# Optimization experiments

Measured on AMD Instinct MI355X. Metric: run time of the kernel, lower is better.

Reference implementation:

```python
import jax, jax.numpy as jnp
import numpy as np

SET_NUM, SET_SIZE, C, H, F, L_LAYERS, N_BLOCKS = 2048, 36, 192, 8, 384, 8, 4
N = SET_NUM * SET_SIZE


def _ln(x, g, b, eps=1e-5):
    m = x.mean(-1, keepdims=True)
    v = ((x - m) ** 2).mean(-1, keepdims=True)
    return (x - m) * jax.lax.rsqrt(v + eps) * g + b


def setup_inputs() -> dict:
    key = jax.random.key(0)
    ks = jax.random.split(key, 32)
    src = jax.random.normal(ks[0], (N, C), dtype=jnp.float32)
    pos_embed = jax.random.normal(ks[1], (2, N, C), dtype=jnp.float32)
    # each (shift, set) index tensor is a permutation of arange(N) -> every voxel appears exactly once
    perms = [jax.random.permutation(ks[2 + j], N).reshape(SET_NUM, SET_SIZE) for j in range(4)]
    set_voxel_inds = jnp.stack([jnp.stack(perms[0:2]), jnp.stack(perms[2:4])]).astype(jnp.int32)
    set_voxel_masks = jnp.zeros((2, 2, SET_NUM, SET_SIZE), dtype=bool)

    def p(k, shape, std=0.02):
        return (jax.random.normal(k, shape) * std).astype(jnp.float32)

    inp = dict(src=src, pos_embed=pos_embed, set_voxel_inds=set_voxel_inds,
               set_voxel_masks=set_voxel_masks,
               in_proj_w=p(ks[6], (L_LAYERS, 3 * C, C)), in_proj_b=p(ks[7], (L_LAYERS, 3 * C)),
               out_w=p(ks[8], (L_LAYERS, C, C)), out_b=p(ks[9], (L_LAYERS, C)),
               lin1_w=p(ks[10], (L_LAYERS, F, C)), lin1_b=p(ks[11], (L_LAYERS, F)),
               lin2_w=p(ks[12], (L_LAYERS, C, F)), lin2_b=p(ks[13], (L_LAYERS, C)),
               ln1_g=jnp.ones((L_LAYERS, C)), ln1_b=jnp.zeros((L_LAYERS, C)),
               ln2_g=jnp.ones((L_LAYERS, C)), ln2_b=jnp.zeros((L_LAYERS, C)),
               enc_g=jnp.ones((L_LAYERS, C)), enc_b=jnp.zeros((L_LAYERS, C)),
               blk_g=jnp.ones((N_BLOCKS, C)), blk_b=jnp.zeros((N_BLOCKS, C)))
    return inp


def reference(src, pos_embed, set_voxel_inds, set_voxel_masks,
              in_proj_w, in_proj_b, out_w, out_b, lin1_w, lin1_b, lin2_w, lin2_b,
              ln1_g, ln1_b, ln2_g, ln2_b, enc_g, enc_b, blk_g, blk_b):
    n_vox = src.shape[0]
    Dh = C // H
    scale = 1.0 / np.sqrt(Dh)

    def set_attn(x, pos, inds, mask, li):
        g = x[inds]                      # (S,K,C) gather voxels into sets
        qk_in = g + pos[inds]
        Wq, Wk, Wv = jnp.split(in_proj_w[li], 3, axis=0)
        bq, bk, bv = jnp.split(in_proj_b[li], 3)
        S, K = inds.shape
        q = (qk_in @ Wq.T + bq).reshape(S, K, H, Dh)
        k = (qk_in @ Wk.T + bk).reshape(S, K, H, Dh)
        v = (g @ Wv.T + bv).reshape(S, K, H, Dh)
        scores = jnp.einsum('skhd,slhd->shkl', q, k) * scale
        scores = jnp.where(mask[:, None, None, :], -1e9, scores)
        attn = jax.nn.softmax(scores, axis=-1)
        o = jnp.einsum('shkl,slhd->skhd', attn, v).reshape(S, K, C)
        o = o @ out_w[li].T + out_b[li]
        # torch.unique + flipped scatter == take the first occurrence of each voxel index
        flat = inds.reshape(-1)
        first = jnp.full((n_vox,), flat.size, dtype=flat.dtype).at[flat].min(
            jnp.arange(flat.size, dtype=flat.dtype))
        src2 = o.reshape(-1, C)[first]
        x = _ln(x + src2, ln1_g[li], ln1_b[li])
        ff = jax.nn.gelu(x @ lin1_w[li].T + lin1_b[li], approximate=False) @ lin2_w[li].T + lin2_b[li]
        x = _ln(x + ff, ln2_g[li], ln2_b[li])
        return x

    out = src
    for block_id in range(N_BLOCKS):
        residual = out
        shift = block_id % 2
        for i in range(2):
            li = block_id * 2 + i
            identity = out
            out = set_attn(out, pos_embed[i], set_voxel_inds[shift, i],
                           set_voxel_masks[shift, i], li)
            out = _ln(out + identity, enc_g[li], enc_b[li])
        out = _ln(out + residual, blk_g[block_id], blk_b[block_id])
    return out
```

## Files before the change

### kernel.cpp

```cpp
#include <hip/hip_runtime.h>
#include <hip/hip_bf16.h>
#include <hip/hip_fp16.h>

#define SETS 2048
#define SS   36
#define CDIM 192
#define HEADS 8
#define DH   24
#define FDIM 384
#define NVOX (SETS*SS)
#define NBLOCKS 4

typedef __hip_bfloat16 bf16;
typedef _Float16 f16;
typedef __attribute__((ext_vector_type(2))) _Float16 h2v;
typedef __attribute__((ext_vector_type(4))) short s4v;
typedef __attribute__((ext_vector_type(8))) short s8v;
typedef __attribute__((ext_vector_type(4))) float f4v;

__device__ __forceinline__ float to_f(float x) { return x; }
__device__ __forceinline__ float to_f(bf16 x)  { return __bfloat162float(x); }

__device__ __forceinline__ short f2bf(float x) {
  bf16 h = __float2bfloat16(x);
  return *reinterpret_cast<short*>(&h);
}
__device__ __forceinline__ unsigned pack2(float a, float b) {
  return ((unsigned)(unsigned short)f2bf(a)) | (((unsigned)(unsigned short)f2bf(b)) << 16);
}

__device__ __forceinline__ float dot2(unsigned a, unsigned b, float acc) {
#if __has_builtin(__builtin_amdgcn_fdot2)
  return __builtin_amdgcn_fdot2(__builtin_bit_cast(h2v, a), __builtin_bit_cast(h2v, b), acc, false);
#else
  h2v ha = __builtin_bit_cast(h2v, a), hb = __builtin_bit_cast(h2v, b);
  return acc + (float)ha[0] * (float)hb[0] + (float)ha[1] * (float)hb[1];
#endif
}
__device__ __forceinline__ unsigned pkh(float a, float b) {
#if __has_builtin(__builtin_amdgcn_cvt_pkrtz)
  return __builtin_bit_cast(unsigned, __builtin_amdgcn_cvt_pkrtz(a, b));
#else
  h2v h; h[0] = (f16)a; h[1] = (f16)b;
  return __builtin_bit_cast(unsigned, h);
#endif
}
__device__ __forceinline__ unsigned permw(unsigned a, unsigned b, unsigned sel) {
#if __has_builtin(__builtin_amdgcn_perm)
  return __builtin_amdgcn_perm(b, a, sel);
#else
  if (sel == 0x05040100u) return (a & 0xffffu) | (b << 16);
  return (a >> 16) | (b & 0xffff0000u);
#endif
}

__device__ __forceinline__ float allreduce64(float v) {
  #pragma unroll
  for (int off = 32; off > 0; off >>= 1) v += __shfl_xor(v, off);
  return v;
}

__device__ __forceinline__ void ln3(float v[3], const float* g, const float* b, int t) {
  float s = allreduce64(v[0] + v[1] + v[2]);
  float m = s * (1.0f / 192.0f);
  float d0 = v[0] - m, d1 = v[1] - m, d2 = v[2] - m;
  float q = allreduce64(d0 * d0 + d1 * d1 + d2 * d2);
  float rs = rsqrtf(q * (1.0f / 192.0f) + 1e-5f);
  v[0] = d0 * rs * g[t]       + b[t];
  v[1] = d1 * rs * g[t + 64]  + b[t + 64];
  v[2] = d2 * rs * g[t + 128] + b[t + 128];
}

__global__ __launch_bounds__(256) void wconv_k(const float* __restrict__ in,
                                               bf16* __restrict__ out, int n8) {
  int i = blockIdx.x * 256 + threadIdx.x;
  if (i < n8) {
    const float4* p = (const float4*)in + (size_t)i * 2;
    float4 a = p[0], b = p[1];
    s8v o;
    o[0] = f2bf(a.x); o[1] = f2bf(a.y); o[2] = f2bf(a.z); o[3] = f2bf(a.w);
    o[4] = f2bf(b.x); o[5] = f2bf(b.y); o[6] = f2bf(b.z); o[7] = f2bf(b.w);
    ((s8v*)out)[i] = o;
  }
}

__global__ __launch_bounds__(256) void init_k(const float* __restrict__ src,
    const float* __restrict__ pos0, float* __restrict__ a0,
    bf16* __restrict__ xb, bf16* __restrict__ xpb) {
  int i = blockIdx.x * 256 + threadIdx.x;
  float4 s = ((const float4*)src)[i];
  float4 p = ((const float4*)pos0)[i];
  ((float4*)a0)[i] = s;
  s4v ob, op;
  ob[0] = f2bf(s.x); ob[1] = f2bf(s.y); ob[2] = f2bf(s.z); ob[3] = f2bf(s.w);
  op[0] = f2bf(s.x + p.x); op[1] = f2bf(s.y + p.y);
  op[2] = f2bf(s.z + p.z); op[3] = f2bf(s.w + p.w);
  ((s4v*)xb)[i]  = ob;
  ((s4v*)xpb)[i] = op;
}

template<typename TO> __device__ __forceinline__ TO fcast(float v);
template<> __device__ __forceinline__ bf16 fcast<bf16>(float v) { return __float2bfloat16(v); }
template<> __device__ __forceinline__ f16  fcast<f16>(float v)  { return (f16)v; }

template<typename TO, int KT, int BM, int BN, int WM, int WN, bool GELU_ACT>
__global__ __launch_bounds__(WM*WN*64) void bgemm_k(
    const bf16* __restrict__ A, const bf16* __restrict__ W,
    const float* __restrict__ bias, TO* __restrict__ Cmat,
    int ldc, int c_off)
{
  constexpr int NTHR = WM * WN * 64;
  constexpr int LD = 40;
  constexpr int MI = BM / (16 * WM);
  constexpr int NJ = BN / (16 * WN);
  constexpr int AC = BM * 4 / NTHR;
  constexpr int BC = BN * 4 / NTHR;
  constexpr int NT = KT / 32;
  static_assert(AC * NTHR == BM * 4 && BC * NTHR == BN * 4, "staging chunks");

  __shared__ short As[2][BM * LD];
  __shared__ short Bs[2][BN * LD];

  const int tid = threadIdx.x;
  const int gx = gridDim.x;
  const int flat = blockIdx.y * gx + blockIdx.x;
  const int chunk = (gx * gridDim.y) >> 3;
  const int work = (flat & 7) * chunk + (flat >> 3);
  const int n0 = (work % gx) * BN;
  const int m0 = (work / gx) * BM;
  const int wave = tid >> 6, lane = tid & 63;
  const int quad = lane >> 4, l16 = lane & 15;
  const int wm = (wave / WN) * (MI * 16);
  const int wn = (wave % WN) * (NJ * 16);

  const bf16* Aptr[AC]; int aoff[AC];
  #pragma unroll
  for (int c = 0; c < AC; c++) {
    int u = tid + c * NTHR;
    int row = u >> 2, c4 = u & 3;
    Aptr[c] = A + (long)(m0 + row) * KT + c4 * 8;
    aoff[c] = row * LD + c4 * 8;
  }
  const bf16* Bptr[BC]; int boff[BC];
  #pragma unroll
  for (int c = 0; c < BC; c++) {
    int u = tid + c * NTHR;
    int row = u >> 2, c4 = u & 3;
    Bptr[c] = W + (long)(n0 + row) * KT + c4 * 8;
    boff[c] = row * LD + c4 * 8;
  }

  uint4 ra[AC], rb[BC];
  #pragma unroll
  for (int c = 0; c < AC; c++) ra[c] = *(const uint4*)(Aptr[c]);
  #pragma unroll
  for (int c = 0; c < BC; c++) rb[c] = *(const uint4*)(Bptr[c]);
  #pragma unroll
  for (int c = 0; c < AC; c++) *(uint4*)&As[0][aoff[c]] = ra[c];
  #pragma unroll
  for (int c = 0; c < BC; c++) *(uint4*)&Bs[0][boff[c]] = rb[c];
  __syncthreads();

  f4v acc[MI][NJ];
  #pragma unroll
  for (int i = 0; i < MI; i++)
    #pragma unroll
    for (int j = 0; j < NJ; j++)
      #pragma unroll
      for (int r = 0; r < 4; r++) acc[i][j][r] = 0.f;

  #pragma unroll
  for (int t = 0; t < NT; t++) {
    const int cur = t & 1;
    if (t + 1 < NT) {
      #pragma unroll
      for (int c = 0; c < AC; c++) ra[c] = *(const uint4*)(Aptr[c] + (t + 1) * 32);
      #pragma unroll
      for (int c = 0; c < BC; c++) rb[c] = *(const uint4*)(Bptr[c] + (t + 1) * 32);
    }
    s8v af[MI], bfv[NJ];
    #pragma unroll
    for (int i = 0; i < MI; i++)
      af[i] = *(const s8v*)&As[cur][(wm + i * 16 + l16) * LD + quad * 8];
    #pragma unroll
    for (int j = 0; j < NJ; j++)
      bfv[j] = *(const s8v*)&Bs[cur][(wn + j * 16 + l16) * LD + quad * 8];
    #pragma unroll
    for (int i = 0; i < MI; i++)
      #pragma unroll
      for (int j = 0; j < NJ; j++)
        acc[i][j] = __builtin_amdgcn_mfma_f32_16x16x32_bf16(af[i], bfv[j], acc[i][j], 0, 0, 0);
    if (t + 1 < NT) {
      #pragma unroll
      for (int c = 0; c < AC; c++) *(uint4*)&As[cur ^ 1][aoff[c]] = ra[c];
      #pragma unroll
      for (int c = 0; c < BC; c++) *(uint4*)&Bs[cur ^ 1][boff[c]] = rb[c];
      __syncthreads();
    }
  }

  #pragma unroll
  for (int j = 0; j < NJ; j++) {
    int gn = n0 + wn + j * 16 + l16;
    float bj = bias[gn];
    #pragma unroll
    for (int i = 0; i < MI; i++) {
      #pragma unroll
      for (int r = 0; r < 4; r++) {
        int gm = m0 + wm + i * 16 + quad * 4 + r;
        float vv = acc[i][j][r] + bj;
        if (GELU_ACT) vv = 0.5f * vv * (1.0f + erff(vv * 0.70710678118654752f));
        Cmat[(long)gm * ldc + c_off + gn] = fcast<TO>(vv);
      }
    }
  }
}

#define KLD 392
__global__ __launch_bounds__(288) void attn_set_k(const f16* __restrict__ qkv,
                                                  const int* __restrict__ inds,
                                                  bf16* __restrict__ o)
{
  __shared__ short kv[SS * KLD];
  __shared__ int si[SS];
  const int s = blockIdx.x;
  const int tid = threadIdx.x;

  if (tid < SS) si[tid] = inds[s * SS + tid];
  __syncthreads();

  const int h = tid / SS;
  const int r = tid - h * SS;
  const int vr = si[r];

  const uint4* qp = (const uint4*)(qkv + (size_t)vr * 576 + h * DH);
  uint4 uq0 = qp[0], uq1 = qp[1], uq2 = qp[2];

  const uint4* gp = (const uint4*)qkv;
  uint4* ls = (uint4*)kv;
  #pragma unroll
  for (int i = 0; i < 6; i++) {
    int u = tid + i * 288;
    int row = u / 48;
    int c = u - row * 48;
    ls[row * 49 + c] = gp[(size_t)si[row] * 72 + 24 + c];
  }
  __syncthreads();

  unsigned qw[12] = { uq0.x, uq0.y, uq0.z, uq0.w,
                      uq1.x, uq1.y, uq1.z, uq1.w,
                      uq2.x, uq2.y, uq2.z, uq2.w };

  const float scale = 0.20412414523193154f;
  float sc[SS];
  #pragma unroll
  for (int l = 0; l < SS; l++) {
    const uint4* kp = (const uint4*)&kv[l * KLD + h * DH];
    uint4 u0 = kp[0], u1 = kp[1], u2 = kp[2];
    float a0 = 0.f, a1 = 0.f, a2 = 0.f;
    a0 = dot2(qw[0], u0.x, a0); a0 = dot2(qw[1], u0.y, a0);
    a0 = dot2(qw[2], u0.z, a0); a0 = dot2(qw[3], u0.w, a0);
    a1 = dot2(qw[4], u1.x, a1); a1 = dot2(qw[5], u1.y, a1);
    a1 = dot2(qw[6], u1.z, a1); a1 = dot2(qw[7], u1.w, a1);
    a2 = dot2(qw[8], u2.x, a2); a2 = dot2(qw[9], u2.y, a2);
    a2 = dot2(qw[10], u2.z, a2); a2 = dot2(qw[11], u2.w, a2);
    sc[l] = (a0 + a1 + a2) * scale;
  }

  float mx = -1e30f;
  #pragma unroll
  for (int l = 0; l < SS; l++) mx = fmaxf(mx, sc[l]);
  float sum = 0.f;
  #pragma unroll
  for (int l = 0; l < SS; l++) { float e = __expf(sc[l] - mx); sc[l] = e; sum += e; }
  float inv = 1.0f / sum;

  float ov[DH];
  #pragma unroll
  for (int d = 0; d < DH; d++) ov[d] = 0.f;
  #pragma unroll
  for (int lp = 0; lp < SS / 2; lp++) {
    const uint4* va = (const uint4*)&kv[(2 * lp) * KLD + 192 + h * DH];
    const uint4* vb = (const uint4*)&kv[(2 * lp + 1) * KLD + 192 + h * DH];
    unsigned pp = pkh(sc[2 * lp], sc[2 * lp + 1]);
    #pragma unroll
    for (int i = 0; i < 3; i++) {
      uint4 ua = va[i], ub = vb[i];
      unsigned wa[4] = { ua.x, ua.y, ua.z, ua.w };
      unsigned wb[4] = { ub.x, ub.y, ub.z, ub.w };
      #pragma unroll
      for (int j = 0; j < 4; j++) {
        unsigned lo = permw(wa[j], wb[j], 0x05040100u);
        unsigned hi = permw(wa[j], wb[j], 0x07060302u);
        ov[8*i + 2*j]     = dot2(pp, lo, ov[8*i + 2*j]);
        ov[8*i + 2*j + 1] = dot2(pp, hi, ov[8*i + 2*j + 1]);
      }
    }
  }

  uint4* op = (uint4*)(o + (size_t)vr * CDIM + h * DH);
  #pragma unroll
  for (int i = 0; i < 3; i++) {
    uint4 u;
    u.x = pack2(ov[8*i+0] * inv, ov[8*i+1] * inv);
    u.y = pack2(ov[8*i+2] * inv, ov[8*i+3] * inv);
    u.z = pack2(ov[8*i+4] * inv, ov[8*i+5] * inv);
    u.w = pack2(ov[8*i+6] * inv, ov[8*i+7] * inv);
    op[i] = u;
  }
}

__global__ __launch_bounds__(256) void ln1_k(
    const float* __restrict__ xin, const bf16* __restrict__ o2,
    const float* __restrict__ g, const float* __restrict__ b,
    float* __restrict__ x1, bf16* __restrict__ x1b)
{
  int p = blockIdx.x * 4 + (threadIdx.x >> 6);
  int t = threadIdx.x & 63;
  long base = (long)p * 192;
  float v[3];
  #pragma unroll
  for (int j = 0; j < 3; j++) { int c = t + 64 * j; v[j] = xin[base + c] + to_f(o2[base + c]); }
  ln3(v, g, b, t);
  #pragma unroll
  for (int j = 0; j < 3; j++) {
    int c = t + 64 * j;
    x1[base + c]  = v[j];
    x1b[base + c] = __float2bfloat16(v[j]);
  }
}

template<bool HAS_BLK, bool WRITE_OUT>
__global__ __launch_bounds__(256) void ln_chain_k(
    const float* __restrict__ x1, const bf16* __restrict__ ff,
    const float* __restrict__ identity, const float* __restrict__ resid,
    const float* __restrict__ g2, const float* __restrict__ b2,
    const float* __restrict__ ge, const float* __restrict__ be,
    const float* __restrict__ gb, const float* __restrict__ bb,
    float* __restrict__ outf, float* __restrict__ outd,
    const float* __restrict__ posn, bf16* __restrict__ xbo,
    bf16* __restrict__ xpo)
{
  int row = blockIdx.x * 4 + (threadIdx.x >> 6);
  int t = threadIdx.x & 63;
  long base = (long)row * 192;
  float v[3];
  #pragma unroll
  for (int j = 0; j < 3; j++) { int c = t + 64 * j; v[j] = x1[base + c] + to_f(ff[base + c]); }
  ln3(v, g2, b2, t);
  #pragma unroll
  for (int j = 0; j < 3; j++) { int c = t + 64 * j; v[j] += identity[base + c]; }
  ln3(v, ge, be, t);
  if (HAS_BLK) {
    #pragma unroll
    for (int j = 0; j < 3; j++) { int c = t + 64 * j; v[j] += resid[base + c]; }
    ln3(v, gb, bb, t);
  }
  #pragma unroll
  for (int j = 0; j < 3; j++) {
    int c = t + 64 * j;
    outf[base + c] = v[j];
    if (WRITE_OUT) outd[base + c] = v[j];
  }
  if (xbo) {
    #pragma unroll
    for (int j = 0; j < 3; j++) { int c = t + 64 * j; xbo[base + c] = __float2bfloat16(v[j]); }
  }
  if (xpo) {
    #pragma unroll
    for (int j = 0; j < 3; j++) {
      int c = t + 64 * j;
      xpo[base + c] = __float2bfloat16(v[j] + posn[base + c]);
    }
  }
}

extern "C" void kernel_launch(void* const* d_in, const int* in_sizes, int n_in,
                              void* d_out, int out_size, void* d_ws, size_t ws_size,
                              hipStream_t stream)
{
  const float* src       = (const float*)d_in[0];
  const float* pos_embed = (const float*)d_in[1];
  const int*   svi       = (const int*)d_in[2];
  const float* ipw  = (const float*)d_in[4];
  const float* ipb  = (const float*)d_in[5];
  const float* outw = (const float*)d_in[6];
  const float* outb = (const float*)d_in[7];
  const float* l1w  = (const float*)d_in[8];
  const float* l1b  = (const float*)d_in[9];
  const float* l2w  = (const float*)d_in[10];
  const float* l2b  = (const float*)d_in[11];
  const float* ln1g = (const float*)d_in[12];
  const float* ln1b = (const float*)d_in[13];
  const float* ln2g = (const float*)d_in[14];
  const float* ln2b = (const float*)d_in[15];
  const float* encg = (const float*)d_in[16];
  const float* encb = (const float*)d_in[17];
  const float* blkg = (const float*)d_in[18];
  const float* blkb = (const float*)d_in[19];

  char* w = (char*)d_ws;
  const size_t ACT  = (size_t)NVOX * CDIM * sizeof(float);
  const size_t QKVB = (size_t)NVOX * 576 * sizeof(f16);
  const size_t OB   = (size_t)NVOX * CDIM * sizeof(bf16);
  float* act[3] = { (float*)w, (float*)(w + ACT), (float*)(w + 2 * ACT) };
  f16*  qkv   = (f16*)(w + 3 * ACT);
  bf16* obuf  = (bf16*)(w + 3 * ACT + QKVB);
  bf16* o2buf = (bf16*)(w + 3 * ACT + QKVB + OB);
  bf16* xb    = o2buf;
  bf16* xpb   = (bf16*)(w + 3 * ACT + QKVB + 2 * OB);
  bf16* wbf   = (bf16*)(w + 3 * ACT + QKVB + 3 * OB);
  bf16* wip_b  = wbf;
  bf16* wout_b = wip_b  + (size_t)8 * 576 * 192;
  bf16* wl1_b  = wout_b + (size_t)8 * 192 * 192;
  bf16* wl2_b  = wl1_b  + (size_t)8 * 384 * 192;
  bf16* hbuf  = (bf16*)qkv;
  bf16* ffbuf = obuf;

  wconv_k<<<(8*576*192/8 + 255)/256, 256, 0, stream>>>(ipw,  wip_b,  8*576*192/8);
  wconv_k<<<(8*192*192/8 + 255)/256, 256, 0, stream>>>(outw, wout_b, 8*192*192/8);
  wconv_k<<<(8*384*192/8 + 255)/256, 256, 0, stream>>>(l1w,  wl1_b,  8*384*192/8);
  wconv_k<<<(8*192*384/8 + 255)/256, 256, 0, stream>>>(l2w,  wl2_b,  8*192*384/8);

  init_k<<<NVOX * CDIM / 4 / 256, 256, 0, stream>>>(src, pos_embed, act[0], xb, xpb);

  int r = 0, ia = 1, ib = 2;
  for (int blkid = 0; blkid < NBLOCKS; blkid++) {
    int shift = blkid & 1;
    float* xres = act[r];
    float* cur  = act[r];
    float* outs[2] = { act[ia], act[ib] };
    for (int i = 0; i < 2; i++) {
      int li = blkid * 2 + i;
      const int* inds = svi + (size_t)(shift * 2 + i) * SETS * SS;
      const float* Bip = ipb + (size_t)li * 576;

      bgemm_k<f16, 192, 128, 128, 2, 2, false>
          <<<dim3(3, NVOX / 128), 256, 0, stream>>>(
          xpb, wip_b + (size_t)li * 576 * 192, Bip, qkv, 576, 0);
      bgemm_k<f16, 192, 128, 64, 4, 1, false>
          <<<dim3(3, NVOX / 128), 256, 0, stream>>>(
          xb, wip_b + (size_t)li * 576 * 192 + (size_t)384 * 192, Bip + 384, qkv,
          576, 384);

      attn_set_k<<<SETS, 288, 0, stream>>>(qkv, inds, obuf);

      bgemm_k<bf16, 192, 128, 64, 4, 1, false>
          <<<dim3(3, NVOX / 128), 256, 0, stream>>>(
          obuf, wout_b + (size_t)li * 192 * 192, outb + (size_t)li * 192, o2buf,
          192, 0);

      float* x1 = outs[i];
      ln1_k<<<NVOX / 4, 256, 0, stream>>>(cur, o2buf,
          ln1g + (size_t)li * 192, ln1b + (size_t)li * 192, x1, xpb );

      bgemm_k<bf16, 192, 128, 128, 2, 2, true>
          <<<dim3(3, NVOX / 128), 256, 0, stream>>>(
          xpb , wl1_b + (size_t)li * 384 * 192, l1b + (size_t)li * 384, hbuf,
          384, 0);
      bgemm_k<bf16, 384, 128, 64, 4, 1, false>
          <<<dim3(3, NVOX / 128), 256, 0, stream>>>(
          hbuf, wl2_b + (size_t)li * 192 * 384, l2b + (size_t)li * 192, ffbuf,
          192, 0);

      bool isFinal = (blkid == NBLOCKS - 1 && i == 1);
      const float* posn = pos_embed + (size_t)((li + 1) & 1) * NVOX * CDIM;
      if (i == 1) {
        if (isFinal)
          ln_chain_k<true, true><<<NVOX / 4, 256, 0, stream>>>(x1, ffbuf, cur, xres,
              ln2g + (size_t)li * 192, ln2b + (size_t)li * 192,
              encg + (size_t)li * 192, encb + (size_t)li * 192,
              blkg + (size_t)blkid * 192, blkb + (size_t)blkid * 192,
              x1, (float*)d_out, nullptr, nullptr, nullptr);
        else
          ln_chain_k<true, false><<<NVOX / 4, 256, 0, stream>>>(x1, ffbuf, cur, xres,
              ln2g + (size_t)li * 192, ln2b + (size_t)li * 192,
              encg + (size_t)li * 192, encb + (size_t)li * 192,
              blkg + (size_t)blkid * 192, blkb + (size_t)blkid * 192,
              x1, nullptr, posn, xb, xpb);
      } else {
        ln_chain_k<false, false><<<NVOX / 4, 256, 0, stream>>>(x1, ffbuf, cur, xres,
            ln2g + (size_t)li * 192, ln2b + (size_t)li * 192,
            encg + (size_t)li * 192, encb + (size_t)li * 192,
            nullptr, nullptr, x1, nullptr, posn, xb, xpb);
      }
      cur = x1;
    }
    int newr = ib, na = r, nb = ia;
    r = newr; ia = na; ib = nb;
  }
}
```

Baseline: 2.446 ms.

## Fuse layernorm chains into out-proj and FFN2 GEMM epilogues

Adds a GEMM kernel whose block covers the full 192-wide output row, so the bias, residual add and one to three layernorms run in the epilogue via 16-lane shuffles. It replaces the out-proj GEMM plus ln1 kernel and the FFN2 GEMM plus the ln-chain kernel. This removes the bf16 intermediate round trips and four launches per layer. In exchange each block holds a 128x192 accumulator, which raises register pressure and lowers occupancy, and the grid shrinks from 3x576 to 576 blocks. The fused path also drops the bf16 rounding of the GEMM output before the layernorm.

```diff
diff --git a/kernel.cpp b/kernel.cpp
--- a/kernel.cpp
+++ b/kernel.cpp
@@ -18,9 +18,6 @@
 typedef __attribute__((ext_vector_type(8))) short s8v;
 typedef __attribute__((ext_vector_type(4))) float f4v;
 
-__device__ __forceinline__ float to_f(float x) { return x; }
-__device__ __forceinline__ float to_f(bf16 x)  { return __bfloat162float(x); }
-
 __device__ __forceinline__ short f2bf(float x) {
   bf16 h = __float2bfloat16(x);
   return *reinterpret_cast<short*>(&h);
@@ -54,21 +51,21 @@
 #endif
 }
 
-__device__ __forceinline__ float allreduce64(float v) {
-  #pragma unroll
-  for (int off = 32; off > 0; off >>= 1) v += __shfl_xor(v, off);
-  return v;
-}
-
-__device__ __forceinline__ void ln3(float v[3], const float* g, const float* b, int t) {
-  float s = allreduce64(v[0] + v[1] + v[2]);
+__device__ __forceinline__ void lnq(float v[12], const float* g, const float* b, int l16) {
+  float s = 0.f;
+  #pragma unroll
+  for (int j = 0; j < 12; j++) s += v[j];
+  #pragma unroll
+  for (int off = 8; off > 0; off >>= 1) s += __shfl_xor(s, off);
   float m = s * (1.0f / 192.0f);
-  float d0 = v[0] - m, d1 = v[1] - m, d2 = v[2] - m;
-  float q = allreduce64(d0 * d0 + d1 * d1 + d2 * d2);
+  float q = 0.f;
+  #pragma unroll
+  for (int j = 0; j < 12; j++) { float d = v[j] - m; q += d * d; }
+  #pragma unroll
+  for (int off = 8; off > 0; off >>= 1) q += __shfl_xor(q, off);
   float rs = rsqrtf(q * (1.0f / 192.0f) + 1e-5f);
-  v[0] = d0 * rs * g[t]       + b[t];
-  v[1] = d1 * rs * g[t + 64]  + b[t + 64];
-  v[2] = d2 * rs * g[t + 128] + b[t + 128];
+  #pragma unroll
+  for (int j = 0; j < 12; j++) v[j] = (v[j] - m) * rs * g[l16 + j * 16] + b[l16 + j * 16];
 }
 
 __global__ __launch_bounds__(256) void wconv_k(const float* __restrict__ in,
@@ -216,6 +213,147 @@
   }
 }
 
+template<int KT, int EPI, bool HAS_BLK, bool WRITE_OUT>
+__global__ __launch_bounds__(256) void bgemm_ln_k(
+    const bf16* __restrict__ A, const bf16* __restrict__ W,
+    const float* __restrict__ bias,
+    const float* __restrict__ xin, const float* __restrict__ identity,
+    const float* __restrict__ resid,
+    const float* __restrict__ g1v, const float* __restrict__ b1v,
+    const float* __restrict__ g2v, const float* __restrict__ b2v,
+    const float* __restrict__ g3v, const float* __restrict__ b3v,
+    const float* __restrict__ posn,
+    float* __restrict__ outf, float* __restrict__ outd,
+    bf16* __restrict__ xbo, bf16* __restrict__ xpo)
+{
+  constexpr int BM = 128, BN = 192, LD = 40, NTHR = 256;
+  constexpr int MI = 2, NJ = 12, AC = 2, BC = 3, NT = KT / 32;
+  __shared__ short As[2][BM * LD];
+  __shared__ short Bs[2][BN * LD];
+  __shared__ float prm[7][192];
+
+  const int tid = threadIdx.x;
+  const int chunk = gridDim.x >> 3;
+  const int flat = blockIdx.x;
+  const int work = (flat & 7) * chunk + (flat >> 3);
+  const int m0 = work * BM;
+  const int wave = tid >> 6, lane = tid & 63;
+  const int quad = lane >> 4, l16 = lane & 15;
+  const int wm = wave * 32;
+
+  if (tid < 192) {
+    prm[0][tid] = bias[tid];
+    prm[1][tid] = g1v[tid]; prm[2][tid] = b1v[tid];
+    if (EPI == 2) {
+      prm[3][tid] = g2v[tid]; prm[4][tid] = b2v[tid];
+      if (HAS_BLK) { prm[5][tid] = g3v[tid]; prm[6][tid] = b3v[tid]; }
+    }
+  }
+
+  const bf16* Aptr[AC]; int aoff[AC];
+  #pragma unroll
+  for (int c = 0; c < AC; c++) {
+    int u = tid + c * NTHR;
+    int row = u >> 2, c4 = u & 3;
+    Aptr[c] = A + (long)(m0 + row) * KT + c4 * 8;
+    aoff[c] = row * LD + c4 * 8;
+  }
+  const bf16* Bptr[BC]; int boff[BC];
+  #pragma unroll
+  for (int c = 0; c < BC; c++) {
+    int u = tid + c * NTHR;
+    int row = u >> 2, c4 = u & 3;
+    Bptr[c] = W + (long)row * KT + c4 * 8;
+    boff[c] = row * LD + c4 * 8;
+  }
+
+  uint4 ra[AC], rb[BC];
+  #pragma unroll
+  for (int c = 0; c < AC; c++) ra[c] = *(const uint4*)(Aptr[c]);
+  #pragma unroll
+  for (int c = 0; c < BC; c++) rb[c] = *(const uint4*)(Bptr[c]);
+  #pragma unroll
+  for (int c = 0; c < AC; c++) *(uint4*)&As[0][aoff[c]] = ra[c];
+  #pragma unroll
+  for (int c = 0; c < BC; c++) *(uint4*)&Bs[0][boff[c]] = rb[c];
+  __syncthreads();
+
+  f4v acc[MI][NJ];
+  #pragma unroll
+  for (int i = 0; i < MI; i++)
+    #pragma unroll
+    for (int j = 0; j < NJ; j++)
+      #pragma unroll
+      for (int r = 0; r < 4; r++) acc[i][j][r] = 0.f;
+
+  #pragma unroll
+  for (int t = 0; t < NT; t++) {
+    const int cur = t & 1;
+    if (t + 1 < NT) {
+      #pragma unroll
+      for (int c = 0; c < AC; c++) ra[c] = *(const uint4*)(Aptr[c] + (t + 1) * 32);
+      #pragma unroll
+      for (int c = 0; c < BC; c++) rb[c] = *(const uint4*)(Bptr[c] + (t + 1) * 32);
+    }
+    s8v af[MI], bfv[NJ];
+    #pragma unroll
+    for (int i = 0; i < MI; i++)
+      af[i] = *(const s8v*)&As[cur][(wm + i * 16 + l16) * LD + quad * 8];
+    #pragma unroll
+    for (int j = 0; j < NJ; j++)
+      bfv[j] = *(const s8v*)&Bs[cur][(j * 16 + l16) * LD + quad * 8];
+    #pragma unroll
+    for (int i = 0; i < MI; i++)
+      #pragma unroll
+      for (int j = 0; j < NJ; j++)
+        acc[i][j] = __builtin_amdgcn_mfma_f32_16x16x32_bf16(af[i], bfv[j], acc[i][j], 0, 0, 0);
+    if (t + 1 < NT) {
+      #pragma unroll
+      for (int c = 0; c < AC; c++) *(uint4*)&As[cur ^ 1][aoff[c]] = ra[c];
+      #pragma unroll
+      for (int c = 0; c < BC; c++) *(uint4*)&Bs[cur ^ 1][boff[c]] = rb[c];
+      __syncthreads();
+    }
+  }
+
+  #pragma unroll
+  for (int i = 0; i < MI; i++) {
+    #pragma unroll
+    for (int r = 0; r < 4; r++) {
+      long rb_ = (long)(m0 + wm + i * 16 + quad * 4 + r) * 192;
+      float v[NJ];
+      #pragma unroll
+      for (int j = 0; j < NJ; j++) {
+        int c = l16 + j * 16;
+        v[j] = acc[i][j][r] + prm[0][c] + xin[rb_ + c];
+      }
+      lnq(v, &prm[1][0], &prm[2][0], l16);
+      if (EPI == 2) {
+        #pragma unroll
+        for (int j = 0; j < NJ; j++) v[j] += identity[rb_ + l16 + j * 16];
+        lnq(v, &prm[3][0], &prm[4][0], l16);
+        if (HAS_BLK) {
+          #pragma unroll
+          for (int j = 0; j < NJ; j++) v[j] += resid[rb_ + l16 + j * 16];
+          lnq(v, &prm[5][0], &prm[6][0], l16);
+        }
+      }
+      #pragma unroll
+      for (int j = 0; j < NJ; j++) {
+        int c = l16 + j * 16;
+        outf[rb_ + c] = v[j];
+        if (WRITE_OUT) outd[rb_ + c] = v[j];
+        if (EPI == 1) {
+          xbo[rb_ + c] = __float2bfloat16(v[j]);
+        } else {
+          if (xbo) xbo[rb_ + c] = __float2bfloat16(v[j]);
+          if (xpo) xpo[rb_ + c] = __float2bfloat16(v[j] + posn[rb_ + c]);
+        }
+      }
+    }
+  }
+}
+
 #define KLD 392
 __global__ __launch_bounds__(288) void attn_set_k(const f16* __restrict__ qkv,
                                                   const int* __restrict__ inds,
@@ -307,71 +445,6 @@
     u.z = pack2(ov[8*i+4] * inv, ov[8*i+5] * inv);
     u.w = pack2(ov[8*i+6] * inv, ov[8*i+7] * inv);
     op[i] = u;
-  }
-}
-
-__global__ __launch_bounds__(256) void ln1_k(
-    const float* __restrict__ xin, const bf16* __restrict__ o2,
-    const float* __restrict__ g, const float* __restrict__ b,
-    float* __restrict__ x1, bf16* __restrict__ x1b)
-{
-  int p = blockIdx.x * 4 + (threadIdx.x >> 6);
-  int t = threadIdx.x & 63;
-  long base = (long)p * 192;
-  float v[3];
-  #pragma unroll
-  for (int j = 0; j < 3; j++) { int c = t + 64 * j; v[j] = xin[base + c] + to_f(o2[base + c]); }
-  ln3(v, g, b, t);
-  #pragma unroll
-  for (int j = 0; j < 3; j++) {
-    int c = t + 64 * j;
-    x1[base + c]  = v[j];
-    x1b[base + c] = __float2bfloat16(v[j]);
-  }
-}
-
-template<bool HAS_BLK, bool WRITE_OUT>
-__global__ __launch_bounds__(256) void ln_chain_k(
-    const float* __restrict__ x1, const bf16* __restrict__ ff,
-    const float* __restrict__ identity, const float* __restrict__ resid,
-    const float* __restrict__ g2, const float* __restrict__ b2,
-    const float* __restrict__ ge, const float* __restrict__ be,
-    const float* __restrict__ gb, const float* __restrict__ bb,
-    float* __restrict__ outf, float* __restrict__ outd,
-    const float* __restrict__ posn, bf16* __restrict__ xbo,
-    bf16* __restrict__ xpo)
-{
-  int row = blockIdx.x * 4 + (threadIdx.x >> 6);
-  int t = threadIdx.x & 63;
-  long base = (long)row * 192;
-  float v[3];
-  #pragma unroll
-  for (int j = 0; j < 3; j++) { int c = t + 64 * j; v[j] = x1[base + c] + to_f(ff[base + c]); }
-  ln3(v, g2, b2, t);
-  #pragma unroll
-  for (int j = 0; j < 3; j++) { int c = t + 64 * j; v[j] += identity[base + c]; }
-  ln3(v, ge, be, t);
-  if (HAS_BLK) {
-    #pragma unroll
-    for (int j = 0; j < 3; j++) { int c = t + 64 * j; v[j] += resid[base + c]; }
-    ln3(v, gb, bb, t);
-  }
-  #pragma unroll
-  for (int j = 0; j < 3; j++) {
-    int c = t + 64 * j;
-    outf[base + c] = v[j];
-    if (WRITE_OUT) outd[base + c] = v[j];
-  }
-  if (xbo) {
-    #pragma unroll
-    for (int j = 0; j < 3; j++) { int c = t + 64 * j; xbo[base + c] = __float2bfloat16(v[j]); }
-  }
-  if (xpo) {
-    #pragma unroll
-    for (int j = 0; j < 3; j++) {
-      int c = t + 64 * j;
-      xpo[base + c] = __float2bfloat16(v[j] + posn[base + c]);
-    }
   }
 }
 
@@ -415,7 +488,6 @@
   bf16* wl1_b  = wout_b + (size_t)8 * 192 * 192;
   bf16* wl2_b  = wl1_b  + (size_t)8 * 384 * 192;
   bf16* hbuf  = (bf16*)qkv;
-  bf16* ffbuf = obuf;
 
   wconv_k<<<(8*576*192/8 + 255)/256, 256, 0, stream>>>(ipw,  wip_b,  8*576*192/8);
   wconv_k<<<(8*192*192/8 + 255)/256, 256, 0, stream>>>(outw, wout_b, 8*192*192/8);
@@ -426,12 +498,12 @@
 
   int r = 0, ia = 1, ib = 2;
   for (int blkid = 0; blkid < NBLOCKS; blkid++) {
-    int shift = blkid & 1;
     float* xres = act[r];
     float* cur  = act[r];
     float* outs[2] = { act[ia], act[ib] };
     for (int i = 0; i < 2; i++) {
       int li = blkid * 2 + i;
+      int shift = blkid & 1;
       const int* inds = svi + (size_t)(shift * 2 + i) * SETS * SS;
       const float* Bip = ipb + (size_t)li * 576;
 
@@ -445,44 +517,46 @@
 
       attn_set_k<<<SETS, 288, 0, stream>>>(qkv, inds, obuf);
 
-      bgemm_k<bf16, 192, 128, 64, 4, 1, false>
-          <<<dim3(3, NVOX / 128), 256, 0, stream>>>(
-          obuf, wout_b + (size_t)li * 192 * 192, outb + (size_t)li * 192, o2buf,
-          192, 0);
-
       float* x1 = outs[i];
-      ln1_k<<<NVOX / 4, 256, 0, stream>>>(cur, o2buf,
-          ln1g + (size_t)li * 192, ln1b + (size_t)li * 192, x1, xpb );
+      bgemm_ln_k<192, 1, false, false><<<NVOX / 128, 256, 0, stream>>>(
+          obuf, wout_b + (size_t)li * 192 * 192, outb + (size_t)li * 192,
+          cur, nullptr, nullptr,
+          ln1g + (size_t)li * 192, ln1b + (size_t)li * 192,
+          nullptr, nullptr, nullptr, nullptr, nullptr,
+          x1, nullptr, xpb , nullptr);
 
       bgemm_k<bf16, 192, 128, 128, 2, 2, true>
           <<<dim3(3, NVOX / 128), 256, 0, stream>>>(
           xpb , wl1_b + (size_t)li * 384 * 192, l1b + (size_t)li * 384, hbuf,
           384, 0);
-      bgemm_k<bf16, 384, 128, 64, 4, 1, false>
-          <<<dim3(3, NVOX / 128), 256, 0, stream>>>(
-          hbuf, wl2_b + (size_t)li * 192 * 384, l2b + (size_t)li * 192, ffbuf,
-          192, 0);
 
       bool isFinal = (blkid == NBLOCKS - 1 && i == 1);
       const float* posn = pos_embed + (size_t)((li + 1) & 1) * NVOX * CDIM;
+      const bf16* Al2 = hbuf;
+      const bf16* Wl2 = wl2_b + (size_t)li * 192 * 384;
+      const float* Bl2 = l2b + (size_t)li * 192;
       if (i == 1) {
         if (isFinal)
-          ln_chain_k<true, true><<<NVOX / 4, 256, 0, stream>>>(x1, ffbuf, cur, xres,
+          bgemm_ln_k<384, 2, true, true><<<NVOX / 128, 256, 0, stream>>>(
+              Al2, Wl2, Bl2, x1, cur, xres,
               ln2g + (size_t)li * 192, ln2b + (size_t)li * 192,
               encg + (size_t)li * 192, encb + (size_t)li * 192,
               blkg + (size_t)blkid * 192, blkb + (size_t)blkid * 192,
-              x1, (float*)d_out, nullptr, nullptr, nullptr);
+              nullptr, x1, (float*)d_out, nullptr, nullptr);
         else
-          ln_chain_k<true, false><<<NVOX / 4, 256, 0, stream>>>(x1, ffbuf, cur, xres,
+          bgemm_ln_k<384, 2, true, false><<<NVOX / 128, 256, 0, stream>>>(
+              Al2, Wl2, Bl2, x1, cur, xres,
               ln2g + (size_t)li * 192, ln2b + (size_t)li * 192,
               encg + (size_t)li * 192, encb + (size_t)li * 192,
               blkg + (size_t)blkid * 192, blkb + (size_t)blkid * 192,
-              x1, nullptr, posn, xb, xpb);
+              posn, x1, nullptr, xb, xpb);
       } else {
-        ln_chain_k<false, false><<<NVOX / 4, 256, 0, stream>>>(x1, ffbuf, cur, xres,
+        bgemm_ln_k<384, 2, false, false><<<NVOX / 128, 256, 0, stream>>>(
+            Al2, Wl2, Bl2, x1, cur, nullptr,
             ln2g + (size_t)li * 192, ln2b + (size_t)li * 192,
             encg + (size_t)li * 192, encb + (size_t)li * 192,
-            nullptr, nullptr, x1, nullptr, posn, xb, xpb);
+            nullptr, nullptr,
+            posn, x1, nullptr, xb, xpb);
       }
       cur = x1;
     }
```

After: 4.095 ms. +67.4%, slower.
